# Performance work log

Measured on AMD Instinct MI355X. Metric: run time of the kernel, lower is better.

The kernel has to match this reference:

```python
import jax, jax.numpy as jnp
import numpy as np

ALPHA = 0.85  # position gain (init kwarg alpha)
BETA = 0.005  # velocity gain (init kwarg beta)


def setup_inputs() -> dict:
    key = jax.random.key(0)
    Z = jax.random.normal(key, (4096, 8192), dtype=jnp.float32)
    return {"Z": Z}


def reference(Z) -> jnp.ndarray:
    # alpha-beta (g-h) filter recurrence, scanned over the time axis.
    #   diff = z - p;  x = p + a*diff;  v += b*diff;  p = x + v
    # Initial state: p = Z[:, 0], v = 0  (so x_0 == Z[:, 0]).
    a = jnp.asarray(ALPHA, Z.dtype)
    b = jnp.asarray(BETA, Z.dtype)

    def step(carry, z):
        p, v = carry
        diff = z - p
        x = p + a * diff
        v = v + b * diff
        p = x + v
        return (p, v), x

    p0 = Z[:, 0]
    v0 = jnp.zeros_like(p0)
    # scan over time: Z.T has shape [T, B]
    _, xs = jax.lax.scan(step, (p0, v0), Z.T)
    return xs.T  # [B, T]
```

## Files before the change

### kernel.cpp

```cpp
#include <hip/hip_runtime.h>


#define A_CONST 0.85f
#define B_CONST 0.005f

typedef float vfloat4 __attribute__((ext_vector_type(4)));

constexpr int ROWS   = 4096;
constexpr int T      = 8192;
constexpr int W      = 4096;
constexpr int L      = 32;
constexpr int NSEC   = T / W;
constexpr int STRIDE = 33;
constexpr int NCHUNK = W / L;

__global__ __launch_bounds__(128, 4)
void kalman_kernel(const float* __restrict__ Z, float* __restrict__ X) {
    const int tid  = threadIdx.x;
    const int wid  = tid >> 6;
    const int lane = tid & 63;
    const int row  = blockIdx.x;

    __shared__ float buf[NCHUNK * STRIDE];
    __shared__ float scr[4];

    const float* Zr = Z + (size_t)row * T;
    float*       Xr = X + (size_t)row * T;

    double m00 = 1.0 - (double)A_CONST - (double)B_CONST, m01 = 1.0;
    double m10 = -(double)B_CONST,                        m11 = 1.0;
    #pragma unroll
    for (int i = 0; i < 5; ++i) {
        double n00 = m00*m00 + m01*m10, n01 = m00*m01 + m01*m11;
        double n10 = m10*m00 + m11*m10, n11 = m10*m01 + m11*m11;
        m00 = n00; m01 = n01; m10 = n10; m11 = n11;
    }
    double g00[7], g01[7], g10[7], g11[7];
    g00[0] = m00; g01[0] = m01; g10[0] = m10; g11[0] = m11;
    #pragma unroll
    for (int k = 1; k < 7; ++k) {
        g00[k] = g00[k-1]*g00[k-1] + g01[k-1]*g10[k-1];
        g01[k] = g00[k-1]*g01[k-1] + g01[k-1]*g11[k-1];
        g10[k] = g10[k-1]*g00[k-1] + g11[k-1]*g10[k-1];
        g11[k] = g10[k-1]*g01[k-1] + g11[k-1]*g11[k-1];
    }
    float sc00[6], sc01[6], sc10[6], sc11[6];
    #pragma unroll
    for (int k = 0; k < 6; ++k) {
        sc00[k] = (float)g00[k]; sc01[k] = (float)g01[k];
        sc10[k] = (float)g10[k]; sc11[k] = (float)g11[k];
    }
    const float w00 = (float)g00[6], w01 = (float)g01[6];
    const float w10 = (float)g10[6], w11 = (float)g11[6];
    double l00 = 1.0, l01 = 0.0, l10 = 0.0, l11 = 1.0;
    #pragma unroll
    for (int k = 0; k < 6; ++k) {
        if ((lane >> k) & 1) {
            double n00 = g00[k]*l00 + g01[k]*l10, n01 = g00[k]*l01 + g01[k]*l11;
            double n10 = g10[k]*l00 + g11[k]*l10, n11 = g10[k]*l01 + g11[k]*l11;
            l00 = n00; l01 = n01; l10 = n10; l11 = n11;
        }
    }
    const float La00 = (float)l00, La01 = (float)l01;
    const float La10 = (float)l10, La11 = (float)l11;

    float ps = Zr[0];
    float vs = 0.0f;

    float4 r[8];
    {
        const float4* src = (const float4*)Zr;
        #pragma unroll
        for (int i = 0; i < 8; ++i) r[i] = src[i * 128 + tid];
    }

    for (int s = 0; s < NSEC; ++s) {
        #pragma unroll
        for (int i = 0; i < 8; ++i) {
            int f = i * 128 + tid;
            int c = f >> 3;
            int j = (f & 7) << 2;
            float* p = buf + c * STRIDE + j;
            p[0] = r[i].x; p[1] = r[i].y; p[2] = r[i].z; p[3] = r[i].w;
        }

        if (s + 1 < NSEC) {
            const float4* src = (const float4*)(Zr + (s + 1) * W);
            #pragma unroll
            for (int i = 0; i < 8; ++i) r[i] = src[i * 128 + tid];
        }

        __syncthreads();

        float c32[L];
        float bp, bv;
        {
            float p = 0.0f, v = 0.0f;
            const float* zc = buf + tid * STRIDE;
            #pragma unroll
            for (int j = 0; j < L; ++j) {
                float z    = zc[j];
                c32[j]     = z;
                float diff = z - p;
                float x    = p + A_CONST * diff;
                v += B_CONST * diff;
                p  = x + v;
            }
            bp = p; bv = v;
        }

        float sb0 = bp, sb1 = bv;
        #pragma unroll
        for (int k = 0; k < 6; ++k) {
            const int d = 1 << k;
            float ob0 = __shfl_up(sb0, d);
            float ob1 = __shfl_up(sb1, d);
            if (lane >= d) {
                sb0 = sc00[k]*ob0 + sc01[k]*ob1 + sb0;
                sb1 = sc10[k]*ob0 + sc11[k]*ob1 + sb1;
            }
        }

        float eb0 = __shfl_up(sb0, 1);
        float eb1 = __shfl_up(sb1, 1);
        if (lane == 0) { eb0 = 0.0f; eb1 = 0.0f; }

        float i0 = __shfl(sb0, 63);
        float i1 = __shfl(sb1, 63);
        if (lane == 0) { scr[wid * 2] = i0; scr[wid * 2 + 1] = i1; }
        __syncthreads();

        const float I00 = scr[0], I01 = scr[1];
        const float I10 = scr[2], I11 = scr[3];

        const float T0 = w00*ps + w01*vs + I00;
        const float T1 = w10*ps + w11*vs + I01;
        const float S0 = wid ? T0 : ps;
        const float S1 = wid ? T1 : vs;
        const float np = w00*T0 + w01*T1 + I10;
        const float nv = w10*T0 + w11*T1 + I11;

        float p = La00*S0 + La01*S1 + eb0;
        float v = La10*S0 + La11*S1 + eb1;

        {
            float* zc = buf + tid * STRIDE;
            #pragma unroll
            for (int j = 0; j < L; ++j) {
                float z    = c32[j];
                float diff = z - p;
                float x    = p + A_CONST * diff;
                v += B_CONST * diff;
                p  = x + v;
                zc[j] = x;
            }
        }

        __syncthreads();

        {
            vfloat4* dst = (vfloat4*)(Xr + s * W);
            #pragma unroll
            for (int i = 0; i < 8; ++i) {
                int f = i * 128 + tid;
                int c = f >> 3;
                int j = (f & 7) << 2;
                const float* q = buf + c * STRIDE + j;
                vfloat4 v4 = { q[0], q[1], q[2], q[3] };
                __builtin_nontemporal_store(v4, dst + f);
            }
        }

        __syncthreads();

        ps = np; vs = nv;
    }
}

extern "C" void kernel_launch(void* const* d_in, const int* in_sizes, int n_in,
                              void* d_out, int out_size, void* d_ws, size_t ws_size,
                              hipStream_t stream) {
    const float* Z = (const float*)d_in[0];
    float*       X = (float*)d_out;
    dim3 grid(ROWS), block(128);
    hipLaunchKernelGGL(kalman_kernel, grid, block, 0, stream, Z, X);
}
```

Before: 45.26 us.

## Assign one wavefront per row and drop LDS staging for register-only scan

Each wavefront now processes one full row in 8 sections of 1024 elements, with 16 elements per lane, instead of two wavefronts sharing a row through an LDS transpose buffer. Loads and stores go straight from contiguous per-lane float4s in registers, which removes the shared-memory buffer, the block barriers and the cross-wave combine. The cost is that each lane's global accesses are strided 64 bytes apart, so per-instruction coalescing is worse, and the nontemporal stores are replaced by plain stores. There are also more sequential sections per row.

```diff
diff --git a/kernel.cpp b/kernel.cpp
--- a/kernel.cpp
+++ b/kernel.cpp
@@ -4,25 +4,17 @@
 #define A_CONST 0.85f
 #define B_CONST 0.005f
 
-typedef float vfloat4 __attribute__((ext_vector_type(4)));
+constexpr int ROWS = 4096;
+constexpr int T    = 8192;
+constexpr int L    = 16;
+constexpr int W    = 64 * L;
+constexpr int NSEC = T / W;
 
-constexpr int ROWS   = 4096;
-constexpr int T      = 8192;
-constexpr int W      = 4096;
-constexpr int L      = 32;
-constexpr int NSEC   = T / W;
-constexpr int STRIDE = 33;
-constexpr int NCHUNK = W / L;
-
-__global__ __launch_bounds__(128, 4)
+__global__ __launch_bounds__(256, 8)
 void kalman_kernel(const float* __restrict__ Z, float* __restrict__ X) {
-    const int tid  = threadIdx.x;
-    const int wid  = tid >> 6;
-    const int lane = tid & 63;
-    const int row  = blockIdx.x;
-
-    __shared__ float buf[NCHUNK * STRIDE];
-    __shared__ float scr[4];
+    const int wid  = threadIdx.x >> 6;
+    const int lane = threadIdx.x & 63;
+    const int row  = (blockIdx.x << 2) | wid;
 
     const float* Zr = Z + (size_t)row * T;
     float*       Xr = X + (size_t)row * T;
@@ -30,7 +22,7 @@
     double m00 = 1.0 - (double)A_CONST - (double)B_CONST, m01 = 1.0;
     double m10 = -(double)B_CONST,                        m11 = 1.0;
     #pragma unroll
-    for (int i = 0; i < 5; ++i) {
+    for (int i = 0; i < 4; ++i) {
         double n00 = m00*m00 + m01*m10, n01 = m00*m01 + m01*m11;
         double n10 = m10*m00 + m11*m10, n11 = m10*m01 + m11*m11;
         m00 = n00; m01 = n01; m10 = n10; m11 = n11;
@@ -52,6 +44,7 @@
     }
     const float w00 = (float)g00[6], w01 = (float)g01[6];
     const float w10 = (float)g10[6], w11 = (float)g11[6];
+
     double l00 = 1.0, l01 = 0.0, l10 = 0.0, l11 = 1.0;
     #pragma unroll
     for (int k = 0; k < 6; ++k) {
@@ -67,44 +60,33 @@
     float ps = Zr[0];
     float vs = 0.0f;
 
-    float4 r[8];
+    float4 rc[4], rn[4];
     {
-        const float4* src = (const float4*)Zr;
+        const float4* src = (const float4*)(Zr + lane * L);
         #pragma unroll
-        for (int i = 0; i < 8; ++i) r[i] = src[i * 128 + tid];
+        for (int i = 0; i < 4; ++i) rc[i] = src[i];
     }
 
     for (int s = 0; s < NSEC; ++s) {
-        #pragma unroll
-        for (int i = 0; i < 8; ++i) {
-            int f = i * 128 + tid;
-            int c = f >> 3;
-            int j = (f & 7) << 2;
-            float* p = buf + c * STRIDE + j;
-            p[0] = r[i].x; p[1] = r[i].y; p[2] = r[i].z; p[3] = r[i].w;
+        if (s + 1 < NSEC) {
+            const float4* src = (const float4*)(Zr + (s + 1) * W + lane * L);
+            #pragma unroll
+            for (int i = 0; i < 4; ++i) rn[i] = src[i];
         }
 
-        if (s + 1 < NSEC) {
-            const float4* src = (const float4*)(Zr + (s + 1) * W);
-            #pragma unroll
-            for (int i = 0; i < 8; ++i) r[i] = src[i * 128 + tid];
-        }
-
-        __syncthreads();
-
-        float c32[L];
         float bp, bv;
         {
             float p = 0.0f, v = 0.0f;
-            const float* zc = buf + tid * STRIDE;
             #pragma unroll
-            for (int j = 0; j < L; ++j) {
-                float z    = zc[j];
-                c32[j]     = z;
-                float diff = z - p;
-                float x    = p + A_CONST * diff;
-                v += B_CONST * diff;
-                p  = x + v;
+            for (int i = 0; i < 4; ++i) {
+                float zv[4] = { rc[i].x, rc[i].y, rc[i].z, rc[i].w };
+                #pragma unroll
+                for (int j = 0; j < 4; ++j) {
+                    float diff = zv[j] - p;
+                    float x    = p + A_CONST * diff;
+                    v += B_CONST * diff;
+                    p  = x + v;
+                }
             }
             bp = p; bv = v;
         }
@@ -120,60 +102,41 @@
                 sb1 = sc10[k]*ob0 + sc11[k]*ob1 + sb1;
             }
         }
-
         float eb0 = __shfl_up(sb0, 1);
         float eb1 = __shfl_up(sb1, 1);
         if (lane == 0) { eb0 = 0.0f; eb1 = 0.0f; }
-
         float i0 = __shfl(sb0, 63);
         float i1 = __shfl(sb1, 63);
-        if (lane == 0) { scr[wid * 2] = i0; scr[wid * 2 + 1] = i1; }
-        __syncthreads();
 
-        const float I00 = scr[0], I01 = scr[1];
-        const float I10 = scr[2], I11 = scr[3];
+        float p   = La00*ps + La01*vs + eb0;
+        float v   = La10*ps + La11*vs + eb1;
+        float nps = w00*ps + w01*vs + i0;
+        float nvs = w10*ps + w11*vs + i1;
 
-        const float T0 = w00*ps + w01*vs + I00;
-        const float T1 = w10*ps + w11*vs + I01;
-        const float S0 = wid ? T0 : ps;
-        const float S1 = wid ? T1 : vs;
-        const float np = w00*T0 + w01*T1 + I10;
-        const float nv = w10*T0 + w11*T1 + I11;
-
-        float p = La00*S0 + La01*S1 + eb0;
-        float v = La10*S0 + La11*S1 + eb1;
-
-        {
-            float* zc = buf + tid * STRIDE;
+        #pragma unroll
+        for (int i = 0; i < 4; ++i) {
+            float zv[4] = { rc[i].x, rc[i].y, rc[i].z, rc[i].w };
+            float xv[4];
             #pragma unroll
-            for (int j = 0; j < L; ++j) {
-                float z    = c32[j];
-                float diff = z - p;
+            for (int j = 0; j < 4; ++j) {
+                float diff = zv[j] - p;
                 float x    = p + A_CONST * diff;
                 v += B_CONST * diff;
                 p  = x + v;
-                zc[j] = x;
+                xv[j] = x;
             }
+            rc[i] = make_float4(xv[0], xv[1], xv[2], xv[3]);
         }
 
-        __syncthreads();
-
         {
-            vfloat4* dst = (vfloat4*)(Xr + s * W);
+            float4* dst = (float4*)(Xr + s * W + lane * L);
             #pragma unroll
-            for (int i = 0; i < 8; ++i) {
-                int f = i * 128 + tid;
-                int c = f >> 3;
-                int j = (f & 7) << 2;
-                const float* q = buf + c * STRIDE + j;
-                vfloat4 v4 = { q[0], q[1], q[2], q[3] };
-                __builtin_nontemporal_store(v4, dst + f);
-            }
+            for (int i = 0; i < 4; ++i) dst[i] = rc[i];
         }
 
-        __syncthreads();
-
-        ps = np; vs = nv;
+        ps = nps; vs = nvs;
+        #pragma unroll
+        for (int i = 0; i < 4; ++i) rc[i] = rn[i];
     }
 }
 
@@ -182,6 +145,6 @@
                               hipStream_t stream) {
     const float* Z = (const float*)d_in[0];
     float*       X = (float*)d_out;
-    dim3 grid(ROWS), block(128);
+    dim3 grid(ROWS / 4), block(256);
     hipLaunchKernelGGL(kalman_kernel, grid, block, 0, stream, Z, X);
 }
```

Measured after the change: 52.83 us. 16.7% more time.

## Use single-wavefront blocks per row to remove barriers and cross-wave combine

Applied to the files above, without the earlier changes.

Each row is now processed by one 64-lane wavefront over four 2048-element sections instead of two wavefronts over two 4096-element sections. This drops every __syncthreads and the shared-memory scratch exchange of the inter-wave carry. The carry-in for the next section now comes straight from the wave-level scan. The trade-off is half the threads per row and twice as many sequential sections, each a serial dependency. It relies on wavefront lockstep for the LDS transposes, with no explicit barrier.

```diff
diff --git a/kernel.cpp b/kernel.cpp
--- a/kernel.cpp
+++ b/kernel.cpp
@@ -8,21 +8,17 @@
 
 constexpr int ROWS   = 4096;
 constexpr int T      = 8192;
-constexpr int W      = 4096;
+constexpr int W      = 2048;
 constexpr int L      = 32;
 constexpr int NSEC   = T / W;
 constexpr int STRIDE = 33;
-constexpr int NCHUNK = W / L;
 
-__global__ __launch_bounds__(128, 4)
+__global__ __launch_bounds__(64)
 void kalman_kernel(const float* __restrict__ Z, float* __restrict__ X) {
-    const int tid  = threadIdx.x;
-    const int wid  = tid >> 6;
-    const int lane = tid & 63;
+    const int lane = threadIdx.x;
     const int row  = blockIdx.x;
 
-    __shared__ float buf[NCHUNK * STRIDE];
-    __shared__ float scr[4];
+    __shared__ float buf[64 * STRIDE];
 
     const float* Zr = Z + (size_t)row * T;
     float*       Xr = X + (size_t)row * T;
@@ -52,6 +48,7 @@
     }
     const float w00 = (float)g00[6], w01 = (float)g01[6];
     const float w10 = (float)g10[6], w11 = (float)g11[6];
+
     double l00 = 1.0, l01 = 0.0, l10 = 0.0, l11 = 1.0;
     #pragma unroll
     for (int k = 0; k < 6; ++k) {
@@ -71,13 +68,13 @@
     {
         const float4* src = (const float4*)Zr;
         #pragma unroll
-        for (int i = 0; i < 8; ++i) r[i] = src[i * 128 + tid];
+        for (int i = 0; i < 8; ++i) r[i] = src[i * 64 + lane];
     }
 
     for (int s = 0; s < NSEC; ++s) {
         #pragma unroll
         for (int i = 0; i < 8; ++i) {
-            int f = i * 128 + tid;
+            int f = i * 64 + lane;
             int c = f >> 3;
             int j = (f & 7) << 2;
             float* p = buf + c * STRIDE + j;
@@ -87,16 +84,14 @@
         if (s + 1 < NSEC) {
             const float4* src = (const float4*)(Zr + (s + 1) * W);
             #pragma unroll
-            for (int i = 0; i < 8; ++i) r[i] = src[i * 128 + tid];
+            for (int i = 0; i < 8; ++i) r[i] = src[i * 64 + lane];
         }
-
-        __syncthreads();
 
         float c32[L];
         float bp, bv;
         {
             float p = 0.0f, v = 0.0f;
-            const float* zc = buf + tid * STRIDE;
+            const float* zc = buf + lane * STRIDE;
             #pragma unroll
             for (int j = 0; j < L; ++j) {
                 float z    = zc[j];
@@ -120,31 +115,19 @@
                 sb1 = sc10[k]*ob0 + sc11[k]*ob1 + sb1;
             }
         }
-
         float eb0 = __shfl_up(sb0, 1);
         float eb1 = __shfl_up(sb1, 1);
         if (lane == 0) { eb0 = 0.0f; eb1 = 0.0f; }
-
         float i0 = __shfl(sb0, 63);
         float i1 = __shfl(sb1, 63);
-        if (lane == 0) { scr[wid * 2] = i0; scr[wid * 2 + 1] = i1; }
-        __syncthreads();
 
-        const float I00 = scr[0], I01 = scr[1];
-        const float I10 = scr[2], I11 = scr[3];
-
-        const float T0 = w00*ps + w01*vs + I00;
-        const float T1 = w10*ps + w11*vs + I01;
-        const float S0 = wid ? T0 : ps;
-        const float S1 = wid ? T1 : vs;
-        const float np = w00*T0 + w01*T1 + I10;
-        const float nv = w10*T0 + w11*T1 + I11;
-
-        float p = La00*S0 + La01*S1 + eb0;
-        float v = La10*S0 + La11*S1 + eb1;
+        float p   = La00*ps + La01*vs + eb0;
+        float v   = La10*ps + La11*vs + eb1;
+        float nps = w00*ps + w01*vs + i0;
+        float nvs = w10*ps + w11*vs + i1;
 
         {
-            float* zc = buf + tid * STRIDE;
+            float* zc = buf + lane * STRIDE;
             #pragma unroll
             for (int j = 0; j < L; ++j) {
                 float z    = c32[j];
@@ -156,13 +139,11 @@
             }
         }
 
-        __syncthreads();
-
         {
             vfloat4* dst = (vfloat4*)(Xr + s * W);
             #pragma unroll
             for (int i = 0; i < 8; ++i) {
-                int f = i * 128 + tid;
+                int f = i * 64 + lane;
                 int c = f >> 3;
                 int j = (f & 7) << 2;
                 const float* q = buf + c * STRIDE + j;
@@ -171,9 +152,7 @@
             }
         }
 
-        __syncthreads();
-
-        ps = np; vs = nv;
+        ps = nps; vs = nvs;
     }
 }
 
@@ -182,6 +161,6 @@
                               hipStream_t stream) {
     const float* Z = (const float*)d_in[0];
     float*       X = (float*)d_out;
-    dim3 grid(ROWS), block(128);
+    dim3 grid(ROWS), block(64);
     hipLaunchKernelGGL(kalman_kernel, grid, block, 0, stream, Z, X);
 }
```

Result: no change. 45.20 us (-0.1%).
